# Performance work log

Hardware: AMD Instinct MI355X
Metric: run time of the kernel (lower is better)

Reference implementation:

```python
import jax, jax.numpy as jnp
import numpy as np

KS = 10       # kernel_size
OUT_N = 10    # pred_frames_num
DCT_N = 10
BN_INV = 1.0 / np.sqrt(1.0 + 1e-5)  # BN eval with running_mean=0, running_var=1


def _get_dct_matrix(N):
    k = np.arange(N)[:, None].astype(np.float64)
    i = np.arange(N)[None, :].astype(np.float64)
    w = np.full((N, 1), np.sqrt(2.0 / N))
    w[0, 0] = np.sqrt(1.0 / N)
    dct_m = w * np.cos(np.pi * (i + 0.5) * k / N)
    idct_m = np.linalg.inv(dct_m)
    return dct_m.astype(np.float32), idct_m.astype(np.float32)


def _conv1d(x, w):
    # x: [B, Cin, L], w: [Cout, Cin, K] -> [B, Cout, L-K+1]
    return jax.lax.conv_general_dilated(x, w, (1,), 'VALID',
                                        dimension_numbers=('NCH', 'OIH', 'NCH'))


def setup_inputs() -> dict:
    keys = iter(jax.random.split(jax.random.key(0), 32))
    def rn(shape, s=0.06):
        return (jax.random.normal(next(keys), shape, jnp.float32) * s)
    d = {}
    d['src'] = jax.random.normal(next(keys), (128, 50, 66), jnp.float32)
    d['convQ_w1'] = rn((256, 66, 6)); d['convQ_w2'] = rn((256, 256, 5))
    d['convK_w1'] = rn((256, 66, 6)); d['convK_w2'] = rn((256, 256, 5))
    d['gc1_w'] = rn((20, 256)); d['gc1_att'] = rn((66, 66)); d['gc1_b'] = rn((256,))
    d['bn1_g'] = 1.0 + rn((16896,), 0.1); d['bn1_b'] = rn((16896,), 0.1)
    d['gcb_w1'] = rn((12, 256, 256)); d['gcb_att1'] = rn((12, 66, 66)); d['gcb_b1'] = rn((12, 256))
    d['gcb_bn1_g'] = 1.0 + rn((12, 16896), 0.1); d['gcb_bn1_b'] = rn((12, 16896), 0.1)
    d['gcb_w2'] = rn((12, 256, 256)); d['gcb_att2'] = rn((12, 66, 66)); d['gcb_b2'] = rn((12, 256))
    d['gcb_bn2_g'] = 1.0 + rn((12, 16896), 0.1); d['gcb_bn2_b'] = rn((12, 16896), 0.1)
    d['gc7_w'] = rn((256, 20)); d['gc7_att'] = rn((66, 66)); d['gc7_b'] = rn((20,))
    return d


def reference(src, convQ_w1, convQ_w2, convK_w1, convK_w2,
              gc1_w, gc1_att, gc1_b, bn1_g, bn1_b,
              gcb_w1, gcb_att1, gcb_b1, gcb_bn1_g, gcb_bn1_b,
              gcb_w2, gcb_att2, gcb_b2, gcb_bn2_g, gcb_bn2_b,
              gc7_w, gc7_att, gc7_b):
    bs, input_n, F = src.shape  # [128, 50, 66]
    dct_np, idct_np = _get_dct_matrix(KS + OUT_N)
    dct_m = jnp.asarray(dct_np)
    idct_m = jnp.asarray(idct_np)

    src_t = jnp.transpose(src, (0, 2, 1))             # [bs, F, T]
    src_key = src_t[:, :, :input_n - OUT_N]           # [bs, F, 40]
    src_query = src_t[:, :, -KS:]                     # [bs, F, 10]

    vn = input_n - KS - OUT_N + 1                     # 31
    vl = KS + OUT_N                                   # 20
    idx = np.arange(vl)[None, :] + np.arange(vn)[:, None]   # [vn, vl]
    src_value = src[:, idx].reshape(bs * vn, vl, F)   # sliding windows
    src_value = jnp.matmul(dct_m[:DCT_N], src_value)  # [bs*vn, 10, F]
    src_value = src_value.reshape(bs, vn, DCT_N, F).transpose(0, 1, 3, 2).reshape(bs, vn, F * DCT_N)

    key = jax.nn.relu(_conv1d(jax.nn.relu(_conv1d(src_key / 1000.0, convK_w1)), convK_w2))    # [bs,256,31]
    query = jax.nn.relu(_conv1d(jax.nn.relu(_conv1d(src_query / 1000.0, convQ_w1)), convQ_w2))  # [bs,256,1]

    score = jnp.matmul(query.transpose(0, 2, 1), key) + 1e-15   # [bs,1,31]
    att = score / jnp.sum(score, axis=2, keepdims=True)
    dct_att = jnp.matmul(att, src_value)[:, 0].reshape(bs, F, DCT_N)  # [bs,66,10]

    idx2 = np.concatenate([np.arange(input_n - KS, input_n), np.full(OUT_N, input_n - 1)])
    input_gcn = src[:, idx2]                                   # [bs,20,66]
    dct_in = jnp.matmul(dct_m[:DCT_N], input_gcn).transpose(0, 2, 1)  # [bs,66,10]
    x = jnp.concatenate([dct_in, dct_att], axis=-1)            # [bs,66,20]

    def gconv(h, A, W, b):
        # support = h @ W ; out = A @ support + b
        return jnp.einsum('nm,bmf->bnf', A, h @ W) + b

    def bn(h, g, b):
        sh = h.shape
        return (h.reshape(sh[0], -1) * (g * BN_INV) + b).reshape(sh)

    y = jnp.tanh(bn(gconv(x, gc1_att, gc1_w, gc1_b), bn1_g, bn1_b))  # [bs,66,256]

    def block(y, p):
        w1, a1, b1, g1, be1, w2, a2, b2, g2, be2 = p
        h = jnp.tanh(bn(gconv(y, a1, w1, b1), g1, be1))
        h = jnp.tanh(bn(gconv(h, a2, w2, b2), g2, be2))
        return h + y, None

    y, _ = jax.lax.scan(block, y, (gcb_w1, gcb_att1, gcb_b1, gcb_bn1_g, gcb_bn1_b,
                                   gcb_w2, gcb_att2, gcb_b2, gcb_bn2_g, gcb_bn2_b))

    y = gconv(y, gc7_att, gc7_w, gc7_b) + x                    # [bs,66,20]
    out_gcn = jnp.matmul(idct_m[:, :DCT_N], y[:, :, :DCT_N].transpose(0, 2, 1))  # [bs,20,66]
    return out_gcn[:, :, None, :]                              # [bs,20,1,66] (itera=1)
```

## Files before the change

### kernel.cpp

```cpp
#include <hip/hip_runtime.h>
#include <hip/hip_bf16.h>


typedef __attribute__((ext_vector_type(8))) short short8;
typedef __attribute__((ext_vector_type(4))) float float4v;
typedef __attribute__((ext_vector_type(4))) unsigned uint4v;

#define BNI 0.9999950000374995f

__device__ __forceinline__ short f2bf(float x){
  unsigned u = __float_as_uint(x);
  unsigned r = (u + 0x7fff + ((u >> 16) & 1)) >> 16;
  return (short)r;
}
__device__ __forceinline__ unsigned pk2(float a, float b){
  unsigned r;
  asm("v_cvt_pk_bf16_f32 %0, %1, %2" : "=v"(r) : "v"(a), "v"(b));
  return r;
}
__device__ __forceinline__ float tanh_f(float x){
  x = fminf(fmaxf(x, -9.f), 9.f);
  float e = __expf(2.f * x);
  return (e - 1.f) * __builtin_amdgcn_rcpf(e + 1.f);
}

__global__ __launch_bounds__(256) void k_prep(
    const float* __restrict__ wK1, const float* __restrict__ wQ1,
    const float* __restrict__ wK2, const float* __restrict__ wQ2,
    const float* __restrict__ gw1, const float* __restrict__ gw2,
    const float* __restrict__ gc1_w,
    const float* __restrict__ gc1_att, const float* __restrict__ att1,
    const float* __restrict__ att2, const float* __restrict__ gc7_att,
    const float* __restrict__ g0, const float* __restrict__ be0, const float* __restrict__ b0,
    const float* __restrict__ g1a, const float* __restrict__ be1a, const float* __restrict__ b1a,
    const float* __restrict__ g2a, const float* __restrict__ be2a, const float* __restrict__ b2a,
    float* __restrict__ dct, short* __restrict__ w1T, short* __restrict__ w2T,
    short* __restrict__ wgT, short* __restrict__ gc1wT, short* __restrict__ aG,
    unsigned* __restrict__ bnP)
{
  __shared__ short tle[64][72];
  int bid = blockIdx.x, tid = threadIdx.x;
  if (bid < 2){
    int t = bid*256 + tid;
    if (t < 400){
      int k = t / 20, i = t % 20;
      double w = (k == 0) ? sqrt(1.0/20.0) : sqrt(2.0/20.0);
      dct[t] = (float)(w * cos(3.14159265358979323846 * (i + 0.5) * k / 20.0));
    }
  } else if (bid < 1026){
    int idx = (bid-2)*256 + tid;
    int f = idx >> 9, k = idx & 511;
    float v = 0.f;
    if (k < 396){
      int h = k / 66, c = k - h*66;
      const float* s = (f < 256) ? wK1 : wQ1;
      v = s[((f & 255)*66 + c)*6 + h];
    }
    w1T[idx] = f2bf(v);
  } else if (bid < 3586){
    int idx = (bid-1026)*256 + tid;
    int f = idx / 1280, k = idx - f*1280;
    int h = k >> 8, c = k & 255;
    const float* s = (f < 256) ? wK2 : wQ2;
    w2T[idx] = f2bf(s[((f & 255)*256 + c)*5 + h]);
  } else if (bid < 3970){
    int q = bid - 3586;
    int l = q >> 4, sub = q & 15;
    int kt = (sub >> 2)*64, ft = (sub & 3)*64;
    const float* s = (l < 12) ? (gw1 + l*65536) : (gw2 + (l-12)*65536);
    int c = tid & 63, r4 = tid >> 6;
    #pragma unroll
    for (int p = 0; p < 16; p++){
      int k = p*4 + r4;
      tle[k][c] = f2bf(s[(kt + k)*256 + ft + c]);
    }
    __syncthreads();
    #pragma unroll
    for (int p = 0; p < 16; p++){
      int f = p*4 + r4;
      wgT[l*65536 + (ft + f)*256 + kt + c] = tle[c][f];
    }
  } else if (bid < 4002){
    int idx = (bid-3970)*256 + tid;
    int f = idx >> 5, k = idx & 31;
    gc1wT[idx] = f2bf(k < 20 ? gc1_w[k*256 + f] : 0.f);
  } else if (bid < 4782){
    int idx = (bid-4002)*256 + tid;
    int li = idx / 7680, r = idx - li*7680;
    int n = r / 96, m = r - n*96;
    const float* Af;
    if (li == 0) Af = gc1_att;
    else if (li == 25) Af = gc7_att;
    else if (li & 1) Af = att1 + ((li-1)>>1)*4356;
    else             Af = att2 + ((li-2)>>1)*4356;
    aG[idx] = f2bf((n < 66 && m < 66) ? Af[n*66 + m] : 0.f);
  } else {
    int idx = (bid-4782)*256 + tid;
    if (idx < 25*16896){
      int li = idx / 16896, r = idx - li*16896;
      int f = r & 255;
      const float *g, *be, *bi;
      if (li == 0){ g = g0; be = be0; bi = b0; }
      else {
        int l = (li - 1) >> 1;
        if (li & 1){ g = g1a + l*16896; be = be1a + l*16896; bi = b1a + l*256; }
        else       { g = g2a + l*16896; be = be2a + l*16896; bi = b2a + l*256; }
      }
      float sc = g[r] * BNI;
      float sh = bi[f] * sc + be[r];
      bnP[idx] = pk2(sc, sh);
    }
  }
}

__global__ __launch_bounds__(256) void k_conv1(const float* __restrict__ src,
    const short* __restrict__ w1T, short* __restrict__ kc1q){
  int b = blockIdx.x, ns = blockIdx.y;
  int f0 = ns*128;
  __shared__ short Aim[48*424];
  __shared__ short Wt[128*72];
  int tid = threadIdx.x;
  for (int idx = tid; idx < 48*424; idx += 256){
    int t = idx / 424, kk = idx - t*424;
    float v = 0.f;
    if (kk < 396 && t < 40){
      int h = kk / 66, c = kk - h*66;
      int row = t + h + ((t >= 35) ? 5 : 0);
      v = src[(b*50 + row)*66 + c] * 1e-3f;
    }
    Aim[idx] = f2bf(v);
  }
  int w = tid >> 6, lane = tid & 63, fl = lane & 15, g = lane >> 4;
  float4v acc[3][2];
  #pragma unroll
  for (int i=0;i<3;i++) for (int n=0;n<2;n++) acc[i][n] = (float4v){0.f,0.f,0.f,0.f};
  for (int kt = 0; kt < 416; kt += 64){
    __syncthreads();
    for (int ch = tid; ch < 128*8; ch += 256){
      int r = ch >> 3, kq = ch & 7;
      *(short8*)&Wt[r*72 + kq*8] = *(const short8*)&w1T[(f0 + r)*512 + kt + kq*8];
    }
    __syncthreads();
    int nst = (416 - kt >= 64) ? 2 : 1;
    for (int s = 0; s < nst; s++){
      int k0 = s*32;
      short8 bfr0 = *(const short8*)&Wt[(w*32 + fl)*72 + k0 + g*8];
      short8 bfr1 = *(const short8*)&Wt[(w*32 + 16 + fl)*72 + k0 + g*8];
      #pragma unroll
      for (int i=0;i<3;i++){
        short8 afr = *(const short8*)&Aim[(i*16 + fl)*424 + kt + k0 + g*8];
        acc[i][0] = __builtin_amdgcn_mfma_f32_16x16x32_bf16(afr, bfr0, acc[i][0], 0,0,0);
        acc[i][1] = __builtin_amdgcn_mfma_f32_16x16x32_bf16(afr, bfr1, acc[i][1], 0,0,0);
      }
    }
  }
  #pragma unroll
  for (int i=0;i<3;i++) for (int n=0;n<2;n++) for (int j=0;j<4;j++){
    int t = i*16 + g*4 + j;
    int f = f0 + w*32 + n*16 + fl;
    float v = fmaxf(acc[i][n][j], 0.f);
    if (t < 35 && f < 256) kc1q[(b*40 + t)*256 + f] = f2bf(v);
    else if (t >= 35 && t < 40 && f >= 256) kc1q[(b*40 + t)*256 + (f - 256)] = f2bf(v);
  }
}

__global__ __launch_bounds__(256) void k_conv2(const short* __restrict__ kc1q,
    const short* __restrict__ w2T, float* __restrict__ key, float* __restrict__ q){
  int b = blockIdx.x, ns = blockIdx.y;
  int f0 = ns*128;
  __shared__ short kcs[40*256];
  __shared__ short Wt[128*136];
  char* kcb = (char*)kcs;
  int tid = threadIdx.x;
  for (int ch = tid; ch < 1280; ch += 256){
    int r = ch >> 5, kq = ch & 31;
    unsigned byte = (unsigned)(r*512 + kq*16) ^ (unsigned)((r & 7) << 4);
    *(short8*)(kcb + byte) = *(const short8*)&kc1q[(b*40 + r)*256 + kq*8];
  }
  int w = tid >> 6, lane = tid & 63, fl = lane & 15, g = lane >> 4;
  float4v acc[2][2];
  #pragma unroll
  for (int i=0;i<2;i++) for (int n=0;n<2;n++) acc[i][n] = (float4v){0.f,0.f,0.f,0.f};
  for (int kt = 0; kt < 1280; kt += 128){
    __syncthreads();
    for (int ch = tid; ch < 128*16; ch += 256){
      int r = ch >> 4, kq = ch & 15;
      *(short8*)&Wt[r*136 + kq*8] = *(const short8*)&w2T[(f0 + r)*1280 + kt + kq*8];
    }
    __syncthreads();
    #pragma unroll
    for (int s = 0; s < 4; s++){
      int k = kt + s*32;
      int h = k >> 8, cb = k & 255;
      short8 bfr0 = *(const short8*)&Wt[(w*32 + fl)*136 + s*32 + g*8];
      short8 bfr1 = *(const short8*)&Wt[(w*32 + 16 + fl)*136 + s*32 + g*8];
      #pragma unroll
      for (int i=0;i<2;i++){
        int t = i*16 + fl;
        int row = t + h + ((t == 31) ? 4 : 0);
        unsigned byte = (unsigned)(row*512 + (cb + g*8)*2) ^ (unsigned)((row & 7) << 4);
        short8 afr = *(const short8*)(kcb + byte);
        acc[i][0] = __builtin_amdgcn_mfma_f32_16x16x32_bf16(afr, bfr0, acc[i][0], 0,0,0);
        acc[i][1] = __builtin_amdgcn_mfma_f32_16x16x32_bf16(afr, bfr1, acc[i][1], 0,0,0);
      }
    }
  }
  #pragma unroll
  for (int i=0;i<2;i++) for (int n=0;n<2;n++) for (int j=0;j<4;j++){
    int t = i*16 + g*4 + j;
    int f = f0 + w*32 + n*16 + fl;
    float v = fmaxf(acc[i][n][j], 0.f);
    if (t < 31 && f < 256) key[(b*31 + t)*256 + f] = v;
    else if (t == 31 && f >= 256) q[b*256 + f - 256] = v;
  }
}


template<int KSTEPS, int KSTRIDE, int MODE>
__device__ __forceinline__ void layer_step(
    const short* __restrict__ Wg,
    const unsigned* __restrict__ bnl, const short* __restrict__ aGl,
    float4v (&y_r)[2][5], int w, int fl, int g,
    const char* __restrict__ yin, char* __restrict__ yout,
    char* __restrict__ tT_c)
{
  const short* wbase = Wg + (w*32 + fl)*KSTRIDE + g*8;
  short8 bw[3][2];
  bw[0][0] = *(const short8*)(wbase);
  bw[0][1] = *(const short8*)(wbase + 16*KSTRIDE);
  if (KSTEPS > 1){
    bw[1][0] = *(const short8*)(wbase + 32);
    bw[1][1] = *(const short8*)(wbase + 16*KSTRIDE + 32);
  }

  float4v acc[5][2];
  #pragma unroll
  for (int i=0;i<5;i++){ acc[i][0]=(float4v){0.f,0.f,0.f,0.f}; acc[i][1]=(float4v){0.f,0.f,0.f,0.f}; }
  __builtin_amdgcn_s_setprio(1);
  #pragma unroll
  for (int ks=0; ks<KSTEPS; ks++){
    if (ks + 2 < KSTEPS){
      bw[(ks+2)%3][0] = *(const short8*)(wbase + (ks+2)*32);
      bw[(ks+2)%3][1] = *(const short8*)(wbase + 16*KSTRIDE + (ks+2)*32);
    }
    #pragma unroll
    for (int i=0;i<5;i++){
      int m = i*16 + fl;
      short8 af = *(const short8*)(yin + m*512 + ((ks*64 + g*16) ^ ((m & 15) << 4)));
      acc[i][0] = __builtin_amdgcn_mfma_f32_16x16x32_bf16(af, bw[ks%3][0], acc[i][0], 0,0,0);
      acc[i][1] = __builtin_amdgcn_mfma_f32_16x16x32_bf16(af, bw[ks%3][1], acc[i][1], 0,0,0);
    }
  }
  __builtin_amdgcn_s_setprio(0);

  short8 bA[5];
  #pragma unroll
  for (int n2=0;n2<5;n2++)
    bA[n2] = *(const short8*)&aGl[(n2*16 + fl)*96 + g*8];

  #pragma unroll
  for (int i=0;i<5;i++){
    int mb = (i*16 + g*4)*2;
    #pragma unroll
    for (int n=0;n<2;n++){
      int f = w*32 + n*16 + fl;
      uint2 u; u.x = pk2(acc[i][n][0], acc[i][n][1]); u.y = pk2(acc[i][n][2], acc[i][n][3]);
      *(uint2*)(tT_c + f*256 + (mb ^ ((f & 15) << 4))) = u;
    }
  }

  float4v a2[2][5];
  #pragma unroll
  for (int i=0;i<2;i++)
    #pragma unroll
    for (int n=0;n<5;n++) a2[i][n] = (float4v){0.f,0.f,0.f,0.f};
  uint4v bnp0[5];
  #pragma unroll
  for (int ks2=0; ks2<3; ks2++){
    __builtin_amdgcn_s_setprio(1);
    #pragma unroll
    for (int i2=0;i2<2;i2++){
      int f = w*32 + i2*16 + fl;
      short8 af = *(const short8*)(tT_c + f*256 + ((ks2*64 + g*16) ^ ((f & 15) << 4)));
      #pragma unroll
      for (int n2=0;n2<5;n2++)
        a2[i2][n2] = __builtin_amdgcn_mfma_f32_16x16x32_bf16(af, bA[n2], a2[i2][n2], 0,0,0);
    }
    __builtin_amdgcn_s_setprio(0);
    if (ks2 == 1){
      #pragma unroll
      for (int n2=0;n2<5;n2++){
        int n = n2*16 + fl; int ns = (n < 66) ? n : 0;
        bnp0[n2] = *(const uint4v*)&bnl[ns*256 + w*32 + g*4];
      }
    }
    if (ks2 < 2){
      #pragma unroll
      for (int n2=0;n2<5;n2++)
        bA[n2] = *(const short8*)&aGl[(n2*16 + fl)*96 + (ks2+1)*32 + g*8];
    }
  }

  uint4v bnp1[5];
  #pragma unroll
  for (int n2=0;n2<5;n2++){
    int n = n2*16 + fl; int ns = (n < 66) ? n : 0;
    bnp1[n2] = *(const uint4v*)&bnl[ns*256 + w*32 + 16 + g*4];
  }
  #pragma unroll
  for (int i2=0;i2<2;i2++){
    #pragma unroll
    for (int n2=0;n2<5;n2++){
      int n = n2*16 + fl;
      bool nok = (n < 66);
      float vv[4];
      #pragma unroll
      for (int j=0;j<4;j++){
        unsigned u = (i2 == 0) ? bnp0[n2][j] : bnp1[n2][j];
        float sc = __uint_as_float((u & 0xffffu) << 16);
        float sh = __uint_as_float(u & 0xffff0000u);
        float v = a2[i2][n2][j]*sc + sh;
        v = tanh_f(v);
        if (MODE == 0) y_r[i2][n2][j] = v;
        if (MODE == 2){ v += y_r[i2][n2][j]; y_r[i2][n2][j] = v; }
        vv[j] = nok ? v : 0.f;
      }
      int fb2 = (w*32 + i2*16 + g*4)*2;
      uint2 u2; u2.x = pk2(vv[0], vv[1]); u2.y = pk2(vv[2], vv[3]);
      *(uint2*)(yout + n*512 + (fb2 ^ ((n & 15) << 4))) = u2;
    }
  }
  __syncthreads();
}

__global__ __launch_bounds__(512) void k_mega(const float* __restrict__ src,
    const float* __restrict__ keyv, const float* __restrict__ qv,
    const short* __restrict__ gc1wT, const short* __restrict__ wgT,
    const short* __restrict__ aG, const unsigned* __restrict__ bnP,
    const float* __restrict__ gc7_w, const float* __restrict__ gc7_b,
    const float* __restrict__ dct, float* __restrict__ out)
{
  __shared__ __align__(16) char ybf_c[81920];
  __shared__ __align__(16) char tT_c[65536];
  __shared__ float xo_l[1320];
  __shared__ float x_l[1320];
  __shared__ float dct_l[400];

  int b = blockIdx.x, tid = threadIdx.x;
  int w = tid >> 6, lane = tid & 63, fl = lane & 15, g = lane >> 4;
  char* ybf0 = ybf_c;
  char* ybf1 = ybf_c + 40960;

  float* scr = (float*)tT_c;

  for (int i = tid; i < 10240; i += 512) ((int*)ybf0)[i] = 0;
  for (int i = tid; i < 400; i += 512) dct_l[i] = dct[i];
  if (tid < 496){
    int v = tid >> 4, p = tid & 15;
    const float* kr = keyv + (b*31 + v)*256 + p*16;
    const float* qr = qv + b*256 + p*16;
    float s = 0.f;
    #pragma unroll
    for (int o = 0; o < 16; o++) s += qr[o] * kr[o];
    scr[v*17 + p] = s;
  }
  __syncthreads();
  if (tid < 31){
    float s = 1e-15f;
    #pragma unroll
    for (int p = 0; p < 16; p++) s += scr[tid*17 + p];
    scr[528 + tid] = s;
  }
  __syncthreads();
  if (tid < 64){
    float v = (tid < 31) ? scr[528 + tid] : 0.f;
    float tot = v;
    for (int off = 32; off; off >>= 1) tot += __shfl_down(tot, off);
    tot = __shfl(tot, 0);
    if (tid < 31) scr[528 + tid] = v / tot;
  }
  __syncthreads();
  for (int idx = tid; idx < 1320; idx += 512){
    int i = idx / 66, f = idx - (idx/66)*66;
    float s = 0.f;
    for (int v = 0; v < 31; v++) s += scr[528 + v] * src[(b*50 + v + i)*66 + f];
    scr[560 + idx] = s;
  }
  __syncthreads();
  for (int idx = tid; idx < 660; idx += 512){
    int f = idx / 10, k = idx - (idx/10)*10;
    float s1 = 0.f, s2 = 0.f;
    #pragma unroll
    for (int i = 0; i < 20; i++){
      float d = dct_l[k*20 + i];
      int tt = (i < 10) ? (40 + i) : 49;
      s1 += d * src[(b*50 + tt)*66 + f];
      s2 += d * scr[560 + i*66 + f];
    }
    x_l[f*20 + k] = s1;
    x_l[f*20 + 10 + k] = s2;
    *(short*)(ybf0 + f*512 + ((2*k) ^ ((f & 15) << 4))) = f2bf(s1);
    *(short*)(ybf0 + f*512 + ((2*(10 + k)) ^ ((f & 15) << 4))) = f2bf(s2);
  }
  __syncthreads();
  for (int i = tid; i < 4096; i += 512) ((float4v*)tT_c)[i] = (float4v){0.f,0.f,0.f,0.f};
  __syncthreads();

  float4v y_r[2][5];

  layer_step<1,32,0>(gc1wT, bnP, aG, y_r, w, fl, g, ybf0, ybf1, tT_c);
  #pragma unroll 1
  for (int l = 0; l < 12; l++){
    layer_step<8,256,1>(wgT + l*65536, bnP + (1+2*l)*16896, aG + (1+2*l)*7680,
                        y_r, w, fl, g, ybf1, ybf0, tT_c);
    layer_step<8,256,2>(wgT + (12+l)*65536, bnP + (2+2*l)*16896, aG + (2+2*l)*7680,
                        y_r, w, fl, g, ybf0, ybf1, tT_c);
  }

  for (int i = tid; i < 2048; i += 512){
    int f = i >> 6, kq = (i & 63)*4;
    float v0=0.f, v1=0.f, v2=0.f, v3=0.f;
    if (f < 20){
      v0 = gc7_w[(kq+0)*20 + f]; v1 = gc7_w[(kq+1)*20 + f];
      v2 = gc7_w[(kq+2)*20 + f]; v3 = gc7_w[(kq+3)*20 + f];
    }
    uint2 u; u.x = pk2(v0, v1); u.y = pk2(v2, v3);
    *(uint2*)(ybf0 + f*512 + ((kq*2) ^ ((f & 15) << 4))) = u;
  }
  __syncthreads();

  float4v at[5][2];
  #pragma unroll
  for (int i=0;i<5;i++){ at[i][0] = (float4v){0.f,0.f,0.f,0.f}; at[i][1] = (float4v){0.f,0.f,0.f,0.f}; }
  #pragma unroll
  for (int ks = 0; ks < 8; ks++){
    short8 bf[2];
    #pragma unroll
    for (int n=0;n<2;n++){
      int f = n*16 + fl;
      bf[n] = *(const short8*)(ybf0 + f*512 + ((ks*64 + g*16) ^ ((f & 15) << 4)));
    }
    #pragma unroll
    for (int i=0;i<5;i++){
      int m = i*16 + fl;
      short8 af = *(const short8*)(ybf1 + m*512 + ((ks*64 + g*16) ^ ((m & 15) << 4)));
      at[i][0] = __builtin_amdgcn_mfma_f32_16x16x32_bf16(af, bf[0], at[i][0], 0,0,0);
      at[i][1] = __builtin_amdgcn_mfma_f32_16x16x32_bf16(af, bf[1], at[i][1], 0,0,0);
    }
  }
  if (w == 0){
    #pragma unroll
    for (int i=0;i<5;i++){
      int mb = (i*16 + g*4)*2;
      #pragma unroll
      for (int n=0;n<2;n++){
        int f = n*16 + fl;
        uint2 u; u.x = pk2(at[i][n][0], at[i][n][1]); u.y = pk2(at[i][n][2], at[i][n][3]);
        *(uint2*)(tT_c + f*256 + (mb ^ ((f & 15) << 4))) = u;
      }
    }
  }
  short8 bAt[15];
  {
    const short* aGt = aG + 25*7680;
    #pragma unroll
    for (int ks=0;ks<3;ks++)
      #pragma unroll
      for (int n2=0;n2<5;n2++)
        bAt[ks*5+n2] = *(const short8*)&aGt[(n2*16 + fl)*96 + ks*32 + g*8];
  }
  __syncthreads();

  float4v a2t[2][5];
  #pragma unroll
  for (int i=0;i<2;i++)
    #pragma unroll
    for (int n=0;n<5;n++) a2t[i][n] = (float4v){0.f,0.f,0.f,0.f};
  #pragma unroll
  for (int ks = 0; ks < 3; ks++){
    #pragma unroll
    for (int i2=0;i2<2;i2++){
      int f = i2*16 + fl;
      short8 af = *(const short8*)(tT_c + f*256 + ((ks*64 + g*16) ^ ((f & 15) << 4)));
      #pragma unroll
      for (int n2=0;n2<5;n2++)
        a2t[i2][n2] = __builtin_amdgcn_mfma_f32_16x16x32_bf16(af, bAt[ks*5+n2], a2t[i2][n2], 0,0,0);
    }
  }
  if (w == 0){
    #pragma unroll
    for (int i2=0;i2<2;i2++){
      #pragma unroll
      for (int n2=0;n2<5;n2++){
        int n = n2*16 + fl;
        #pragma unroll
        for (int j=0;j<4;j++){
          int f = i2*16 + g*4 + j;
          if (f < 20 && n < 66)
            xo_l[n*20 + f] = a2t[i2][n2][j] + gc7_b[f] + x_l[n*20 + f];
        }
      }
    }
  }
  __syncthreads();

  for (int idx = tid; idx < 1320; idx += 512){
    int r = idx / 66, fn = idx % 66;
    float s = 0.f;
    #pragma unroll
    for (int k = 0; k < 10; k++) s += dct_l[k*20 + r] * xo_l[fn*20 + k];
    out[(b*20 + r)*66 + fn] = s;
  }
}

extern "C" void kernel_launch(void* const* d_in, const int* in_sizes, int n_in,
                              void* d_out, int out_size, void* d_ws, size_t ws_size,
                              hipStream_t stream) {
  const float* src      = (const float*)d_in[0];
  const float* convQ_w1 = (const float*)d_in[1];
  const float* convQ_w2 = (const float*)d_in[2];
  const float* convK_w1 = (const float*)d_in[3];
  const float* convK_w2 = (const float*)d_in[4];
  const float* gc1_w    = (const float*)d_in[5];
  const float* gc1_att  = (const float*)d_in[6];
  const float* gc1_b    = (const float*)d_in[7];
  const float* bn1_g    = (const float*)d_in[8];
  const float* bn1_b    = (const float*)d_in[9];
  const float* gcb_w1   = (const float*)d_in[10];
  const float* gcb_att1 = (const float*)d_in[11];
  const float* gcb_b1   = (const float*)d_in[12];
  const float* gcb_bn1g = (const float*)d_in[13];
  const float* gcb_bn1b = (const float*)d_in[14];
  const float* gcb_w2   = (const float*)d_in[15];
  const float* gcb_att2 = (const float*)d_in[16];
  const float* gcb_b2   = (const float*)d_in[17];
  const float* gcb_bn2g = (const float*)d_in[18];
  const float* gcb_bn2b = (const float*)d_in[19];
  const float* gc7_w    = (const float*)d_in[20];
  const float* gc7_att  = (const float*)d_in[21];
  const float* gc7_b    = (const float*)d_in[22];
  float* out = (float*)d_out;

  float* ws    = (float*)d_ws;
  float* dct   = ws;
  short* wgT   = (short*)(ws + 333312);
  short* gc1wT = (short*)(ws + 1119744);
  short* w1T   = (short*)(ws + 1123840);
  short* w2T   = (short*)(ws + 1254912);
  short* kc1q  = (short*)(ws + 1582592);
  float* key   = ws + 2237952;
  float* q     = ws + 3253760;
  unsigned* bnP= (unsigned*)(ws + 3290624);
  short* aG    = (short*)(ws + 3713024);

  k_prep<<<6432, 256, 0, stream>>>(convK_w1, convQ_w1, convK_w2, convQ_w2,
      gcb_w1, gcb_w2, gc1_w,
      gc1_att, gcb_att1, gcb_att2, gc7_att,
      bn1_g, bn1_b, gc1_b, gcb_bn1g, gcb_bn1b, gcb_b1,
      gcb_bn2g, gcb_bn2b, gcb_b2,
      dct, w1T, w2T, wgT, gc1wT, aG, bnP);

  k_conv1<<<dim3(128,4), 256, 0, stream>>>(src, w1T, kc1q);
  k_conv2<<<dim3(128,4), 256, 0, stream>>>(kc1q, w2T, key, q);

  k_mega<<<128, 512, 0, stream>>>(src, key, q, gc1wT, wgT, aG, bnP,
      gc7_w, gc7_b, dct, out);
}
```

Before: 277.1 us.

## Fuse both key/query conv stages into the mega kernel using shared memory

Removes the separate conv1 and conv2 kernels and computes both convolutions inside k_mega per batch element. Intermediates (kc1q, key, q) now live in LDS buffers that were already allocated, instead of making round trips through global memory, and two kernel launches are removed. In exchange, the conv work now runs on only 128 blocks of 512 threads instead of 512 blocks each, with weights read straight from global/L2 without LDS staging. The serial work per block before the GCN stages therefore grows.

```diff
diff --git a/kernel.cpp b/kernel.cpp
--- a/kernel.cpp
+++ b/kernel.cpp
@@ -113,108 +113,6 @@
   }
 }
 
-__global__ __launch_bounds__(256) void k_conv1(const float* __restrict__ src,
-    const short* __restrict__ w1T, short* __restrict__ kc1q){
-  int b = blockIdx.x, ns = blockIdx.y;
-  int f0 = ns*128;
-  __shared__ short Aim[48*424];
-  __shared__ short Wt[128*72];
-  int tid = threadIdx.x;
-  for (int idx = tid; idx < 48*424; idx += 256){
-    int t = idx / 424, kk = idx - t*424;
-    float v = 0.f;
-    if (kk < 396 && t < 40){
-      int h = kk / 66, c = kk - h*66;
-      int row = t + h + ((t >= 35) ? 5 : 0);
-      v = src[(b*50 + row)*66 + c] * 1e-3f;
-    }
-    Aim[idx] = f2bf(v);
-  }
-  int w = tid >> 6, lane = tid & 63, fl = lane & 15, g = lane >> 4;
-  float4v acc[3][2];
-  #pragma unroll
-  for (int i=0;i<3;i++) for (int n=0;n<2;n++) acc[i][n] = (float4v){0.f,0.f,0.f,0.f};
-  for (int kt = 0; kt < 416; kt += 64){
-    __syncthreads();
-    for (int ch = tid; ch < 128*8; ch += 256){
-      int r = ch >> 3, kq = ch & 7;
-      *(short8*)&Wt[r*72 + kq*8] = *(const short8*)&w1T[(f0 + r)*512 + kt + kq*8];
-    }
-    __syncthreads();
-    int nst = (416 - kt >= 64) ? 2 : 1;
-    for (int s = 0; s < nst; s++){
-      int k0 = s*32;
-      short8 bfr0 = *(const short8*)&Wt[(w*32 + fl)*72 + k0 + g*8];
-      short8 bfr1 = *(const short8*)&Wt[(w*32 + 16 + fl)*72 + k0 + g*8];
-      #pragma unroll
-      for (int i=0;i<3;i++){
-        short8 afr = *(const short8*)&Aim[(i*16 + fl)*424 + kt + k0 + g*8];
-        acc[i][0] = __builtin_amdgcn_mfma_f32_16x16x32_bf16(afr, bfr0, acc[i][0], 0,0,0);
-        acc[i][1] = __builtin_amdgcn_mfma_f32_16x16x32_bf16(afr, bfr1, acc[i][1], 0,0,0);
-      }
-    }
-  }
-  #pragma unroll
-  for (int i=0;i<3;i++) for (int n=0;n<2;n++) for (int j=0;j<4;j++){
-    int t = i*16 + g*4 + j;
-    int f = f0 + w*32 + n*16 + fl;
-    float v = fmaxf(acc[i][n][j], 0.f);
-    if (t < 35 && f < 256) kc1q[(b*40 + t)*256 + f] = f2bf(v);
-    else if (t >= 35 && t < 40 && f >= 256) kc1q[(b*40 + t)*256 + (f - 256)] = f2bf(v);
-  }
-}
-
-__global__ __launch_bounds__(256) void k_conv2(const short* __restrict__ kc1q,
-    const short* __restrict__ w2T, float* __restrict__ key, float* __restrict__ q){
-  int b = blockIdx.x, ns = blockIdx.y;
-  int f0 = ns*128;
-  __shared__ short kcs[40*256];
-  __shared__ short Wt[128*136];
-  char* kcb = (char*)kcs;
-  int tid = threadIdx.x;
-  for (int ch = tid; ch < 1280; ch += 256){
-    int r = ch >> 5, kq = ch & 31;
-    unsigned byte = (unsigned)(r*512 + kq*16) ^ (unsigned)((r & 7) << 4);
-    *(short8*)(kcb + byte) = *(const short8*)&kc1q[(b*40 + r)*256 + kq*8];
-  }
-  int w = tid >> 6, lane = tid & 63, fl = lane & 15, g = lane >> 4;
-  float4v acc[2][2];
-  #pragma unroll
-  for (int i=0;i<2;i++) for (int n=0;n<2;n++) acc[i][n] = (float4v){0.f,0.f,0.f,0.f};
-  for (int kt = 0; kt < 1280; kt += 128){
-    __syncthreads();
-    for (int ch = tid; ch < 128*16; ch += 256){
-      int r = ch >> 4, kq = ch & 15;
-      *(short8*)&Wt[r*136 + kq*8] = *(const short8*)&w2T[(f0 + r)*1280 + kt + kq*8];
-    }
-    __syncthreads();
-    #pragma unroll
-    for (int s = 0; s < 4; s++){
-      int k = kt + s*32;
-      int h = k >> 8, cb = k & 255;
-      short8 bfr0 = *(const short8*)&Wt[(w*32 + fl)*136 + s*32 + g*8];
-      short8 bfr1 = *(const short8*)&Wt[(w*32 + 16 + fl)*136 + s*32 + g*8];
-      #pragma unroll
-      for (int i=0;i<2;i++){
-        int t = i*16 + fl;
-        int row = t + h + ((t == 31) ? 4 : 0);
-        unsigned byte = (unsigned)(row*512 + (cb + g*8)*2) ^ (unsigned)((row & 7) << 4);
-        short8 afr = *(const short8*)(kcb + byte);
-        acc[i][0] = __builtin_amdgcn_mfma_f32_16x16x32_bf16(afr, bfr0, acc[i][0], 0,0,0);
-        acc[i][1] = __builtin_amdgcn_mfma_f32_16x16x32_bf16(afr, bfr1, acc[i][1], 0,0,0);
-      }
-    }
-  }
-  #pragma unroll
-  for (int i=0;i<2;i++) for (int n=0;n<2;n++) for (int j=0;j<4;j++){
-    int t = i*16 + g*4 + j;
-    int f = f0 + w*32 + n*16 + fl;
-    float v = fmaxf(acc[i][n][j], 0.f);
-    if (t < 31 && f < 256) key[(b*31 + t)*256 + f] = v;
-    else if (t == 31 && f >= 256) q[b*256 + f - 256] = v;
-  }
-}
-
 
 template<int KSTEPS, int KSTRIDE, int MODE>
 __device__ __forceinline__ void layer_step(
@@ -334,7 +232,7 @@
 }
 
 __global__ __launch_bounds__(512) void k_mega(const float* __restrict__ src,
-    const float* __restrict__ keyv, const float* __restrict__ qv,
+    const short* __restrict__ w1T, const short* __restrict__ w2T,
     const short* __restrict__ gc1wT, const short* __restrict__ wgT,
     const short* __restrict__ aG, const unsigned* __restrict__ bnP,
     const float* __restrict__ gc7_w, const float* __restrict__ gc7_b,
@@ -351,14 +249,101 @@
   char* ybf0 = ybf_c;
   char* ybf1 = ybf_c + 40960;
 
+  short* Aim = (short*)ybf1;
+  for (int idx = tid; idx < 48*424; idx += 512){
+    int t = idx / 424, kk = idx - t*424;
+    float v = 0.f;
+    if (kk < 396 && t < 40){
+      int h = kk / 66, c = kk - h*66;
+      int row = t + h + ((t >= 35) ? 5 : 0);
+      v = src[(b*50 + row)*66 + c] * 1e-3f;
+    }
+    Aim[idx] = f2bf(v);
+  }
+  for (int i = tid; i < 400; i += 512) dct_l[i] = dct[i];
+  __syncthreads();
+  {
+    float4v c1[3][4];
+    #pragma unroll
+    for (int i=0;i<3;i++)
+      #pragma unroll
+      for (int n=0;n<4;n++) c1[i][n] = (float4v){0.f,0.f,0.f,0.f};
+    for (int kt = 0; kt < 13; kt++){
+      short8 bw1[4];
+      #pragma unroll
+      for (int n=0;n<4;n++)
+        bw1[n] = *(const short8*)&w1T[(w*64 + n*16 + fl)*512 + kt*32 + g*8];
+      #pragma unroll
+      for (int i=0;i<3;i++){
+        short8 af = *(const short8*)&Aim[(i*16 + fl)*424 + kt*32 + g*8];
+        #pragma unroll
+        for (int n=0;n<4;n++)
+          c1[i][n] = __builtin_amdgcn_mfma_f32_16x16x32_bf16(af, bw1[n], c1[i][n], 0,0,0);
+      }
+    }
+    #pragma unroll
+    for (int i=0;i<3;i++)
+      #pragma unroll
+      for (int n=0;n<4;n++)
+        #pragma unroll
+        for (int j=0;j<4;j++){
+          int t = i*16 + g*4 + j;
+          int f = w*64 + n*16 + fl;
+          float v = fmaxf(c1[i][n][j], 0.f);
+          if (t < 35 && f < 256)
+            *(short*)(ybf0 + t*512 + ((2*f) ^ ((t & 7) << 4))) = f2bf(v);
+          else if (t >= 35 && t < 40 && f >= 256)
+            *(short*)(ybf0 + t*512 + ((2*(f - 256)) ^ ((t & 7) << 4))) = f2bf(v);
+        }
+  }
+  __syncthreads();
+
+  {
+    float4v c2[2][4];
+    #pragma unroll
+    for (int i=0;i<2;i++)
+      #pragma unroll
+      for (int n=0;n<4;n++) c2[i][n] = (float4v){0.f,0.f,0.f,0.f};
+    for (int ks = 0; ks < 40; ks++){
+      short8 bw2[4];
+      #pragma unroll
+      for (int n=0;n<4;n++)
+        bw2[n] = *(const short8*)&w2T[(w*64 + n*16 + fl)*1280 + ks*32 + g*8];
+      int k = ks*32 + g*8;
+      int h = k >> 8, cb = k & 255;
+      #pragma unroll
+      for (int i=0;i<2;i++){
+        int t = i*16 + fl;
+        int row = t + h + ((t == 31) ? 4 : 0);
+        short8 af = *(const short8*)(ybf0 + row*512 + ((2*cb) ^ ((row & 7) << 4)));
+        #pragma unroll
+        for (int n=0;n<4;n++)
+          c2[i][n] = __builtin_amdgcn_mfma_f32_16x16x32_bf16(af, bw2[n], c2[i][n], 0,0,0);
+      }
+    }
+    float* keyq = (float*)ybf1;
+    #pragma unroll
+    for (int i=0;i<2;i++)
+      #pragma unroll
+      for (int n=0;n<4;n++)
+        #pragma unroll
+        for (int j=0;j<4;j++){
+          int t = i*16 + g*4 + j;
+          int f = w*64 + n*16 + fl;
+          float v = fmaxf(c2[i][n][j], 0.f);
+          if (t < 31 && f < 256) keyq[t*256 + f] = v;
+          else if (t == 31 && f >= 256) keyq[7936 + f - 256] = v;
+        }
+  }
+  __syncthreads();
+
   float* scr = (float*)tT_c;
-
+  const float* keyq = (const float*)ybf1;
   for (int i = tid; i < 10240; i += 512) ((int*)ybf0)[i] = 0;
-  for (int i = tid; i < 400; i += 512) dct_l[i] = dct[i];
   if (tid < 496){
     int v = tid >> 4, p = tid & 15;
-    const float* kr = keyv + (b*31 + v)*256 + p*16;
-    const float* qr = qv + b*256 + p*16;
+    const float* kr = keyq + v*256 + p*16;
+    const float* qr = keyq + 7936 + p*16;
     float s = 0.f;
     #pragma unroll
     for (int o = 0; o < 16; o++) s += qr[o] * kr[o];
@@ -547,9 +532,6 @@
   short* gc1wT = (short*)(ws + 1119744);
   short* w1T   = (short*)(ws + 1123840);
   short* w2T   = (short*)(ws + 1254912);
-  short* kc1q  = (short*)(ws + 1582592);
-  float* key   = ws + 2237952;
-  float* q     = ws + 3253760;
   unsigned* bnP= (unsigned*)(ws + 3290624);
   short* aG    = (short*)(ws + 3713024);
 
@@ -560,9 +542,6 @@
       gcb_bn2g, gcb_bn2b, gcb_b2,
       dct, w1T, w2T, wgT, gc1wT, aG, bnP);
 
-  k_conv1<<<dim3(128,4), 256, 0, stream>>>(src, w1T, kc1q);
-  k_conv2<<<dim3(128,4), 256, 0, stream>>>(kc1q, w2T, key, q);
-
-  k_mega<<<128, 512, 0, stream>>>(src, key, q, gc1wT, wgT, aG, bnP,
+  k_mega<<<128, 512, 0, stream>>>(src, w1T, w2T, gc1wT, wgT, aG, bnP,
       gc7_w, gc7_b, dct, out);
 }
```

Measured after the change: 283.8 us. 1.02x slower.
